# Optimization experiments

Hardware: AMD Instinct MI355X
Metric: run time of the kernel (lower is better)

The kernel has to match this reference:

```python
import jax, jax.numpy as jnp
import numpy as np

B, R, C, E = 4, 32, 512, 512
H = 8
D = E // H  # 64
EPS = 1e-6


def setup_inputs() -> dict:
    key = jax.random.key(0)
    ks = jax.random.split(key, 9)
    s = 1.0 / np.sqrt(E)  # keep activations in a sane range
    return {
        "x": jax.random.normal(ks[0], (B, R, C, E), jnp.float32),
        "Wq": jax.random.normal(ks[1], (E, E), jnp.float32) * s,
        "bq": jax.random.normal(ks[2], (E,), jnp.float32) * 0.01,
        "Wk": jax.random.normal(ks[3], (E, E), jnp.float32) * s,
        "bk": jax.random.normal(ks[4], (E,), jnp.float32) * 0.01,
        "Wv": jax.random.normal(ks[5], (E, E), jnp.float32) * s,
        "bv": jax.random.normal(ks[6], (E,), jnp.float32) * 0.01,
        "Wo": jax.random.normal(ks[7], (E, E), jnp.float32) * s,
        "bo": jax.random.normal(ks[8], (E,), jnp.float32) * 0.01,
    }


def reference(x, Wq, bq, Wk, bk, Wv, bv, Wo, bo):
    b, r, c, e = x.shape
    # projections (torch Linear: y = x @ W.T + b), split heads -> [b,r,c,H,D]
    q = (x @ Wq.T + bq).reshape(b, r, c, H, D)
    k = (x @ Wk.T + bk).reshape(b, r, c, H, D)
    v = (x @ Wv.T + bv).reshape(b, r, c, H, D)
    # ELU+1 feature map (Performer/linear attention)
    q = jax.nn.elu(q) + 1.0
    k = jax.nn.elu(k) + 1.0
    # K^T V accumulation over the column axis: [b,r,H,D,D]
    ktv = jnp.einsum('brchd,brche->brhde', k, v)
    # normalizer: q . sum_c(k)  -> [b,r,c,H]
    ksum = k.sum(axis=2)  # [b,r,H,D]
    z = 1.0 / (jnp.einsum('brchd,brhd->brch', q, ksum) + EPS)
    # O(N) attention output: [b,r,c,H,D]
    out_h = jnp.einsum('brchd,brhde->brche', q, ktv) * z[..., None]
    out = out_h.reshape(b, r, c, e)
    return out @ Wo.T + bo
```

## Files before the change

kernel.cpp:

```cpp
#include <hip/hip_runtime.h>

typedef unsigned short u16;
typedef short short8 __attribute__((ext_vector_type(8)));
typedef float f32x4 __attribute__((ext_vector_type(4)));

__device__ __forceinline__ u16 f2b(float f) {
  unsigned u = __float_as_uint(f);
  u = u + 0x7FFFu + ((u >> 16) & 1u);
  return (u16)(u >> 16);
}
__device__ __forceinline__ float b2f(u16 b) {
  return __uint_as_float(((unsigned)b) << 16);
}

#define ASYNC_LD16(g, l)                                                                   \
  __builtin_amdgcn_global_load_lds((const __attribute__((address_space(1))) void*)(g),     \
                                   (__attribute__((address_space(3))) void*)(l), 16, 0, 0)

#define BAR()                                  \
  do {                                         \
    asm volatile("" ::: "memory");             \
    __builtin_amdgcn_s_barrier();              \
    asm volatile("" ::: "memory");             \
  } while (0)

__global__ void convert_x(const float* __restrict__ x, u16* __restrict__ xb) {
  size_t i = ((size_t)blockIdx.x * 256 + threadIdx.x) * 4;
  float4 f = *(const float4*)(x + i);
  ushort4 o;
  o.x = f2b(f.x); o.y = f2b(f.y); o.z = f2b(f.z); o.w = f2b(f.w);
  *(ushort4*)(xb + i) = o;
}

__global__ void convert_w(const float* __restrict__ Wq, const float* __restrict__ Wk,
                          const float* __restrict__ Wv, const float* __restrict__ Wo,
                          u16* __restrict__ Wqkv, u16* __restrict__ Wob) {
  int idx = (blockIdx.x * 256 + threadIdx.x) * 4;
  int row = idx >> 9;
  int col = idx & 511;
  const float* src = (row < 512)    ? Wq + (size_t)row * 512
                     : (row < 1024) ? Wk + (size_t)(row - 512) * 512
                     : (row < 1536) ? Wv + (size_t)(row - 1024) * 512
                                    : Wo + (size_t)(row - 1536) * 512;
  u16* dst = (row < 1536) ? Wqkv + (size_t)row * 512 : Wob + (size_t)(row - 1536) * 512;
  float4 f = *(const float4*)(src + col);
  ushort4 o;
  o.x = f2b(f.x); o.y = f2b(f.y); o.z = f2b(f.z); o.w = f2b(f.w);
  *(ushort4*)(dst + col) = o;
}


#define LDSV(off) (*(const short8*)&S[(off)])

#define STG(gp, scol, dst)                              \
  do {                                                  \
    ASYNC_LD16((gp) + (scol), S + (dst));               \
    ASYNC_LD16((gp) + (scol) + 4096, S + (dst) + 512);  \
  } while (0)

#define MFMA_CL(MB, JB)                                                                     \
  do {                                                                                      \
    __builtin_amdgcn_s_setprio(1);                                                          \
    _Pragma("unroll") for (int m_ = 0; m_ < 4; ++m_)                                        \
      _Pragma("unroll") for (int j_ = 0; j_ < 2; ++j_) {                                    \
        acc[(MB) + m_][(JB) + j_] = __builtin_amdgcn_mfma_f32_16x16x32_bf16(                \
            aq[m_][0], bf[(JB) + j_][0], acc[(MB) + m_][(JB) + j_], 0, 0, 0);               \
        acc[(MB) + m_][(JB) + j_] = __builtin_amdgcn_mfma_f32_16x16x32_bf16(                \
            aq[m_][1], bf[(JB) + j_][1], acc[(MB) + m_][(JB) + j_], 0, 0, 0);               \
      }                                                                                     \
    __builtin_amdgcn_s_setprio(0);                                                          \
  } while (0)

#define KSTEP(BUF, SG1, SG2, SG3, SG4, BND)                                                  \
  do {                                                                                       \
    short8 aq[4][2], bf[4][2];                                                               \
                                                \
    _Pragma("unroll") for (int m_ = 0; m_ < 4; ++m_) {                                       \
      aq[m_][0] = LDSV((BUF) + rA0 + m_ * 1024);                                             \
      aq[m_][1] = LDSV((BUF) + rA1 + m_ * 1024);                                             \
    }                                                                                        \
    _Pragma("unroll") for (int j_ = 0; j_ < 2; ++j_) {                                       \
      bf[j_][0] = LDSV((BUF) + rB0 + j_ * 1024);                                             \
      bf[j_][1] = LDSV((BUF) + rB1 + j_ * 1024);                                             \
    }                                                                                        \
    SG1;                                                                                     \
    BAR(); MFMA_CL(0, 0); BAR();                                                             \
                                                                    \
    _Pragma("unroll") for (int j_ = 0; j_ < 2; ++j_) {                                       \
      bf[2 + j_][0] = LDSV((BUF) + rB0 + (2 + j_) * 1024);                                   \
      bf[2 + j_][1] = LDSV((BUF) + rB1 + (2 + j_) * 1024);                                   \
    }                                                                                        \
    SG2; BAR(); MFMA_CL(0, 2); BAR();                                                        \
                                  \
    _Pragma("unroll") for (int m_ = 0; m_ < 4; ++m_) {                                       \
      aq[m_][0] = LDSV((BUF) + rA0 + (4 + m_) * 1024);                                       \
      aq[m_][1] = LDSV((BUF) + rA1 + (4 + m_) * 1024);                                       \
    }                                                                                        \
    SG3; BAR(); MFMA_CL(4, 2); BAR();                                                        \
                                                                           \
    SG4; BAR(); MFMA_CL(4, 0); BND; BAR();                                                   \
  } while (0)

#define GEMM8_LOOP()                                                                         \
  STG(gB0, 0, dB0); STG(gB1, 0, dB1);                                                        \
  STG(gA0, 0, dA0); STG(gA1, 0, dA1);                                                        \
  STG(gB0, 64, 32768 + dB0); STG(gB1, 64, 32768 + dB1);                                      \
  asm volatile("s_waitcnt vmcnt(4)" ::: "memory");                                           \
  BAR();                                                                                     \
  _Pragma("unroll") for (int i = 0; i < 4; ++i) {                                            \
    const int s1c = (2 * i + 1) * 64, s2c = (2 * i + 2) * 64, s3c = (2 * i + 3) * 64;        \
    if (i < 3) {                                                                             \
      KSTEP(0,                                                                               \
            STG(gA0, s1c, 32768 + dA0),                                                      \
            STG(gA1, s1c, 32768 + dA1),                                                      \
            STG(gB0, s2c, dB0),                                                              \
            STG(gB1, s2c, dB1),                                                              \
            asm volatile("s_waitcnt vmcnt(4)" ::: "memory"));                                \
      KSTEP(32768,                                                                           \
            STG(gA0, s2c, dA0),                                                              \
            STG(gA1, s2c, dA1),                                                              \
            STG(gB0, s3c, 32768 + dB0),                                                      \
            STG(gB1, s3c, 32768 + dB1),                                                      \
            asm volatile("s_waitcnt vmcnt(4)" ::: "memory"));                                \
    } else {                                                                                 \
      KSTEP(0,                                                                               \
            STG(gA0, s1c, 32768 + dA0),                                                      \
            STG(gA1, s1c, 32768 + dA1),                                                      \
            (void)0, (void)0,                                                                \
            asm volatile("s_waitcnt vmcnt(0)" ::: "memory"));                                \
      KSTEP(32768, (void)0, (void)0, (void)0, (void)0, (void)0);                             \
    }                                                                                        \
  }

__global__ __launch_bounds__(512, 2) void gemm_qkv(
    const u16* __restrict__ xb, const u16* __restrict__ Wqkv,
    const float* __restrict__ bq, const float* __restrict__ bk,
    const float* __restrict__ bv, u16* __restrict__ Qb,
    u16* __restrict__ Ktg, u16* __restrict__ Vtg) {
  __shared__ u16 S[65536];
  const int tid = threadIdx.x;
  const int bid = blockIdx.x;
  const int wg = (bid & 7) * 192 + (bid >> 3);
  const int mtile = wg / 6;
  const int ntile = wg - mtile * 6;
  const int blockM = mtile << 8;
  const int blockN = ntile << 8;

  const int lane = tid & 63;
  const int w = tid >> 6;
  const int wm = (w >> 2) << 7;
  const int wn = (w & 3) << 6;
  const int lr = lane & 15;
  const int qd = lane >> 4;
  const int r7 = lr & 7;
  const int l8 = lane >> 3;
  const int l7 = lane & 7;

  const int gsw8 = (l7 ^ l8) * 8;
  const u16* gA0 = xb + (size_t)(blockM + w * 16 + l8) * 512 + gsw8;
  const u16* gA1 = gA0 + 128 * 512;
  const u16* gB0 = Wqkv + (size_t)(blockN + w * 16 + l8) * 512 + gsw8;
  const u16* gB1 = gB0 + 128 * 512;
  const int dA0 = (w * 16 + l8) * 64 + l7 * 8;
  const int dA1 = dA0 + 8192;
  const int dB0 = dA0 + 16384;
  const int dB1 = dA0 + 24576;

  const int rA0 = (wm + lr) * 64 + ((qd) ^ r7) * 8;
  const int rA1 = (wm + lr) * 64 + ((qd + 4) ^ r7) * 8;
  const int rB0 = 16384 + (wn + lr) * 64 + ((qd) ^ r7) * 8;
  const int rB1 = 16384 + (wn + lr) * 64 + ((qd + 4) ^ r7) * 8;

  f32x4 acc[8][4];
#pragma unroll
  for (int m = 0; m < 8; ++m)
#pragma unroll
    for (int j = 0; j < 4; ++j) acc[m][j] = {0.f, 0.f, 0.f, 0.f};

  GEMM8_LOOP();

  const int which = blockN >> 9;
  const int cb = blockN & 511;
  if (which == 0) {
#pragma unroll
    for (int j = 0; j < 4; ++j) {
      int col = cb + wn + j * 16 + lr;
      float bsv = bq[col];
#pragma unroll
      for (int m = 0; m < 8; ++m) {
        int row = blockM + wm + m * 16 + qd * 4;
#pragma unroll
        for (int r = 0; r < 4; ++r) {
          float v = acc[m][j][r] + bsv;
          v = (v > 0.f) ? v + 1.f : __expf(v);
          Qb[(size_t)(row + r) * 512 + col] = f2b(v);
        }
      }
    }
  } else {
    u16* dstT = (which == 1) ? Ktg : Vtg;
    const float* bias = (which == 1) ? bk : bv;
    const int br = blockM >> 9;
    const int t0 = (blockM & 511) + wm;
#pragma unroll
    for (int j = 0; j < 4; ++j) {
      int col = cb + wn + j * 16 + lr;
      float bsv = bias[col];
      size_t rowbase = (size_t)br * 262144 + (size_t)col * 512;
#pragma unroll
      for (int m = 0; m < 8; ++m) {
        int c0 = t0 + m * 16 + qd * 4;
        float v0 = acc[m][j][0] + bsv, v1 = acc[m][j][1] + bsv;
        float v2 = acc[m][j][2] + bsv, v3 = acc[m][j][3] + bsv;
        if (which == 1) {
          v0 = (v0 > 0.f) ? v0 + 1.f : __expf(v0);
          v1 = (v1 > 0.f) ? v1 + 1.f : __expf(v1);
          v2 = (v2 > 0.f) ? v2 + 1.f : __expf(v2);
          v3 = (v3 > 0.f) ? v3 + 1.f : __expf(v3);
        }
        ushort4 p;
        p.x = f2b(v0); p.y = f2b(v1); p.z = f2b(v2); p.w = f2b(v3);
        *(ushort4*)&dstT[rowbase + c0] = p;
      }
    }
  }
}

__global__ void attn(const u16* __restrict__ Qb, const u16* __restrict__ Ktg,
                     const u16* __restrict__ Vtg, u16* __restrict__ Hb) {
  __shared__ u16 KtS[64 * 32];
  __shared__ u16 VtS[64 * 32];
  __shared__ u16 QS[2 * 128 * 32];
  __shared__ u16 ktvT[2 * 64 * 32];
  __shared__ float part[256];
  __shared__ float ksumf[64];
  __shared__ float zs[128];

  const int tid = threadIdx.x;
  const int br = blockIdx.x >> 3;
  const int h = blockIdx.x & 7;
  const int h64 = h * 64;
  const size_t tok0 = (size_t)br * 512;
  const size_t tbase = (size_t)br * 262144 + (size_t)h64 * 512;

  const int lane = tid & 63;
  const int w = tid >> 6;
  const int lr = lane & 15;
  const int qd = lane >> 4;

  const int sc_chan = tid >> 2, sc_seg = tid & 3;

  f32x4 acc[4];
#pragma unroll
  for (int j = 0; j < 4; ++j) acc[j] = {0.f, 0.f, 0.f, 0.f};
  float ks = 0.f;

  for (int ct = 0; ct < 16; ++ct) {
    __syncthreads();
    {
      size_t g = tbase + (size_t)sc_chan * 512 + ct * 32 + sc_seg * 8;
      ASYNC_LD16(Ktg + g, KtS + tid * 8);
      ASYNC_LD16(Vtg + g, VtS + tid * 8);
    }
    __syncthreads();
    short8 a = *(const short8*)&KtS[(w * 16 + lr) * 32 + qd * 8];
#pragma unroll
    for (int j = 0; j < 4; ++j) {
      short8 b = *(const short8*)&VtS[(j * 16 + lr) * 32 + qd * 8];
      acc[j] = __builtin_amdgcn_mfma_f32_16x16x32_bf16(a, b, acc[j], 0, 0, 0);
    }
    ushort4 k0 = *(const ushort4*)&KtS[sc_chan * 32 + sc_seg * 8];
    ushort4 k1 = *(const ushort4*)&KtS[sc_chan * 32 + sc_seg * 8 + 4];
    ks += b2f(k0.x) + b2f(k0.y) + b2f(k0.z) + b2f(k0.w)
        + b2f(k1.x) + b2f(k1.y) + b2f(k1.z) + b2f(k1.w);
  }
  part[tid] = ks;
  {
    int kc = w >> 1;
    int dp = (w & 1) * 16 + qd * 4;
#pragma unroll
    for (int j = 0; j < 4; ++j) {
      int e = j * 16 + lr;
      ushort4 p;
      p.x = f2b(acc[j][0]); p.y = f2b(acc[j][1]);
      p.z = f2b(acc[j][2]); p.w = f2b(acc[j][3]);
      *(ushort4*)&ktvT[kc * 2048 + e * 32 + dp] = p;
    }
  }
  __syncthreads();
  if (tid < 64)
    ksumf[tid] = part[tid * 4] + part[tid * 4 + 1] + part[tid * 4 + 2] + part[tid * 4 + 3];
  __syncthreads();

  short8 bfr[4][2];
#pragma unroll
  for (int j = 0; j < 4; ++j)
#pragma unroll
    for (int kc = 0; kc < 2; ++kc)
      bfr[j][kc] = *(const short8*)&ktvT[kc * 2048 + (j * 16 + lr) * 32 + qd * 8];

  for (int ct = 0; ct < 4; ++ct) {
    __syncthreads();
#pragma unroll
    for (int kc = 0; kc < 2; ++kc)
#pragma unroll
      for (int half = 0; half < 2; ++half)
        ASYNC_LD16(Qb + (tok0 + ct * 128 + half * 64 + sc_chan) * 512 + h64 + kc * 32 + sc_seg * 8,
                   QS + kc * 4096 + half * 2048 + tid * 8);
    __syncthreads();
    if (tid < 128) {
      float s = 0.f;
#pragma unroll 8
      for (int i = 0; i < 32; ++i) {
        int ix = (i + tid) & 31;
        s += b2f(QS[tid * 32 + ix]) * ksumf[ix];
        s += b2f(QS[4096 + tid * 32 + ix]) * ksumf[32 + ix];
      }
      zs[tid] = 1.f / (s + 1e-6f);
    }
    __syncthreads();
#pragma unroll
    for (int s = 0; s < 2; ++s) {
      int mrow = (w * 2 + s) * 16 + lr;
      short8 a0 = *(const short8*)&QS[mrow * 32 + qd * 8];
      short8 a1 = *(const short8*)&QS[4096 + mrow * 32 + qd * 8];
      f32x4 o[4];
#pragma unroll
      for (int j = 0; j < 4; ++j) {
        o[j] = {0.f, 0.f, 0.f, 0.f};
        o[j] = __builtin_amdgcn_mfma_f32_16x16x32_bf16(a0, bfr[j][0], o[j], 0, 0, 0);
        o[j] = __builtin_amdgcn_mfma_f32_16x16x32_bf16(a1, bfr[j][1], o[j], 0, 0, 0);
      }
      int tl = (w * 2 + s) * 16 + qd * 4;
      float z0 = zs[tl], z1 = zs[tl + 1], z2 = zs[tl + 2], z3 = zs[tl + 3];
      size_t gb = (tok0 + ct * 128 + tl) * 512 + h64;
#pragma unroll
      for (int j = 0; j < 4; ++j) {
        int e = j * 16 + lr;
        Hb[gb + e] = f2b(o[j][0] * z0);
        Hb[gb + 512 + e] = f2b(o[j][1] * z1);
        Hb[gb + 1024 + e] = f2b(o[j][2] * z2);
        Hb[gb + 1536 + e] = f2b(o[j][3] * z3);
      }
    }
  }
}

__global__ __launch_bounds__(512, 2) void gemm_out(
    const u16* __restrict__ Hb, const u16* __restrict__ Wob,
    const float* __restrict__ bo, float* __restrict__ out) {
  __shared__ u16 S[65536];
  const int tid = threadIdx.x;
  const int bid = blockIdx.x;
  const int wg = (bid & 7) * 64 + (bid >> 3);
  const int mtile = wg >> 1;
  const int ntile = wg & 1;
  const int blockM = mtile << 8;
  const int blockN = ntile << 8;

  const int lane = tid & 63;
  const int w = tid >> 6;
  const int wm = (w >> 2) << 7;
  const int wn = (w & 3) << 6;
  const int lr = lane & 15;
  const int qd = lane >> 4;
  const int r7 = lr & 7;
  const int l8 = lane >> 3;
  const int l7 = lane & 7;

  const int gsw8 = (l7 ^ l8) * 8;
  const u16* gA0 = Hb + (size_t)(blockM + w * 16 + l8) * 512 + gsw8;
  const u16* gA1 = gA0 + 128 * 512;
  const u16* gB0 = Wob + (size_t)(blockN + w * 16 + l8) * 512 + gsw8;
  const u16* gB1 = gB0 + 128 * 512;
  const int dA0 = (w * 16 + l8) * 64 + l7 * 8;
  const int dA1 = dA0 + 8192;
  const int dB0 = dA0 + 16384;
  const int dB1 = dA0 + 24576;

  const int rA0 = (wm + lr) * 64 + ((qd) ^ r7) * 8;
  const int rA1 = (wm + lr) * 64 + ((qd + 4) ^ r7) * 8;
  const int rB0 = 16384 + (wn + lr) * 64 + ((qd) ^ r7) * 8;
  const int rB1 = 16384 + (wn + lr) * 64 + ((qd + 4) ^ r7) * 8;

  f32x4 acc[8][4];
#pragma unroll
  for (int m = 0; m < 8; ++m)
#pragma unroll
    for (int j = 0; j < 4; ++j) acc[m][j] = {0.f, 0.f, 0.f, 0.f};

  GEMM8_LOOP();

#pragma unroll
  for (int j = 0; j < 4; ++j) {
    int col = blockN + wn + j * 16 + lr;
    float bsv = bo[col];
#pragma unroll
    for (int m = 0; m < 8; ++m) {
      int row = blockM + wm + m * 16 + qd * 4;
#pragma unroll
      for (int r = 0; r < 4; ++r)
        out[(size_t)(row + r) * 512 + col] = acc[m][j][r] + bsv;
    }
  }
}

extern "C" void kernel_launch(void* const* d_in, const int* in_sizes, int n_in,
                              void* d_out, int out_size, void* d_ws, size_t ws_size,
                              hipStream_t stream) {
  const float* x  = (const float*)d_in[0];
  const float* Wq = (const float*)d_in[1];
  const float* bq = (const float*)d_in[2];
  const float* Wk = (const float*)d_in[3];
  const float* bk = (const float*)d_in[4];
  const float* Wv = (const float*)d_in[5];
  const float* bv = (const float*)d_in[6];
  const float* Wo = (const float*)d_in[7];
  const float* bo = (const float*)d_in[8];
  float* out = (float*)d_out;

  char* ws = (char*)d_ws;
  u16* xb   = (u16*)(ws);
  u16* Wqkv = (u16*)(ws + 0x04000000ull);
  u16* Wob  = (u16*)(ws + 0x04200000ull);
  u16* Qb   = (u16*)(ws + 0x04400000ull);
  u16* Ktg  = (u16*)(ws + 0x08400000ull);
  u16* Vtg  = (u16*)(ws + 0x0C400000ull);
  u16* Hb   = xb;

  hipLaunchKernelGGL(convert_x, dim3(32768), dim3(256), 0, stream, x, xb);
  hipLaunchKernelGGL(convert_w, dim3(1024), dim3(256), 0, stream, Wq, Wk, Wv, Wo, Wqkv, Wob);
  hipLaunchKernelGGL(gemm_qkv, dim3(1536), dim3(512), 0, stream, xb, Wqkv, bq, bk, bv, Qb, Ktg, Vtg);
  hipLaunchKernelGGL(attn, dim3(1024), dim3(256), 0, stream, Qb, Ktg, Vtg, Hb);
  hipLaunchKernelGGL(gemm_out, dim3(512), dim3(512), 0, stream, Hb, Wob, bo, out);
}
```

Before: 465.6 us.

## Pipeline attn kernel: double-buffered V, register-direct K/Q loads, MFMA ksum

Rewrites the attention kernel's K^T V phase. V tiles are now double-buffered in LDS with an XOR swizzle and 64-column chunks, K fragments are loaded straight from global into registers with prefetch, and the K column sum is computed by an MFMA against a ones vector. This replaces the old scalar sum, partial-sum array and two barriers per 32-column step. The Q phase drops LDS staging: Q fragments are loaded directly into registers with prefetch, and the normalizer dot product is done with wave shuffles, removing the per-tile syncthreads. The aim is to cut barrier count and LDS traffic and to overlap global loads with MFMA work. In exchange, the kernel uses more registers and issues uncoalesced direct global loads for K and Q.

```diff
diff --git a/kernel.cpp b/kernel.cpp
--- a/kernel.cpp
+++ b/kernel.cpp
@@ -74,7 +74,6 @@
 #define KSTEP(BUF, SG1, SG2, SG3, SG4, BND)                                                  \
   do {                                                                                       \
     short8 aq[4][2], bf[4][2];                                                               \
-                                                \
     _Pragma("unroll") for (int m_ = 0; m_ < 4; ++m_) {                                       \
       aq[m_][0] = LDSV((BUF) + rA0 + m_ * 1024);                                             \
       aq[m_][1] = LDSV((BUF) + rA1 + m_ * 1024);                                             \
@@ -85,19 +84,16 @@
     }                                                                                        \
     SG1;                                                                                     \
     BAR(); MFMA_CL(0, 0); BAR();                                                             \
-                                                                    \
     _Pragma("unroll") for (int j_ = 0; j_ < 2; ++j_) {                                       \
       bf[2 + j_][0] = LDSV((BUF) + rB0 + (2 + j_) * 1024);                                   \
       bf[2 + j_][1] = LDSV((BUF) + rB1 + (2 + j_) * 1024);                                   \
     }                                                                                        \
     SG2; BAR(); MFMA_CL(0, 2); BAR();                                                        \
-                                  \
     _Pragma("unroll") for (int m_ = 0; m_ < 4; ++m_) {                                       \
       aq[m_][0] = LDSV((BUF) + rA0 + (4 + m_) * 1024);                                       \
       aq[m_][1] = LDSV((BUF) + rA1 + (4 + m_) * 1024);                                       \
     }                                                                                        \
     SG3; BAR(); MFMA_CL(4, 2); BAR();                                                        \
-                                                                           \
     SG4; BAR(); MFMA_CL(4, 0); BND; BAR();                                                   \
   } while (0)
 
@@ -226,15 +222,13 @@
   }
 }
 
-__global__ void attn(const u16* __restrict__ Qb, const u16* __restrict__ Ktg,
-                     const u16* __restrict__ Vtg, u16* __restrict__ Hb) {
-  __shared__ u16 KtS[64 * 32];
-  __shared__ u16 VtS[64 * 32];
-  __shared__ u16 QS[2 * 128 * 32];
+__global__ __launch_bounds__(256) void attn(const u16* __restrict__ Qb,
+                                            const u16* __restrict__ Ktg,
+                                            const u16* __restrict__ Vtg,
+                                            u16* __restrict__ Hb) {
+  __shared__ u16 VtS[2][4096];
   __shared__ u16 ktvT[2 * 64 * 32];
-  __shared__ float part[256];
   __shared__ float ksumf[64];
-  __shared__ float zs[128];
 
   const int tid = threadIdx.x;
   const int br = blockIdx.x >> 3;
@@ -248,33 +242,68 @@
   const int lr = lane & 15;
   const int qd = lane >> 4;
 
-  const int sc_chan = tid >> 2, sc_seg = tid & 3;
+  const int sgi = (tid & 7) ^ ((tid >> 3) & 7);
+  const u16* gV = Vtg + tbase + (size_t)(tid >> 3) * 512 + sgi * 8;
+
+#define STGV(buf, ct)                                              \
+  do {                                                             \
+    ASYNC_LD16(gV + (ct) * 64, &VtS[buf][tid * 8]);                \
+    ASYNC_LD16(gV + 16384 + (ct) * 64, &VtS[buf][2048 + tid * 8]); \
+  } while (0)
+
+  const int g0 = ((qd) ^ (lane & 7)) * 8;
+  const int g1 = ((qd + 4) ^ (lane & 7)) * 8;
+
+  const u16* gK = Ktg + tbase + (size_t)(w * 16 + lr) * 512 + qd * 8;
+
+  short8 ones;
+#pragma unroll
+  for (int i = 0; i < 8; ++i) ones[i] = (short)0x3F80;
 
   f32x4 acc[4];
+  f32x4 aks = {0.f, 0.f, 0.f, 0.f};
 #pragma unroll
   for (int j = 0; j < 4; ++j) acc[j] = {0.f, 0.f, 0.f, 0.f};
-  float ks = 0.f;
-
-  for (int ct = 0; ct < 16; ++ct) {
-    __syncthreads();
-    {
-      size_t g = tbase + (size_t)sc_chan * 512 + ct * 32 + sc_seg * 8;
-      ASYNC_LD16(Ktg + g, KtS + tid * 8);
-      ASYNC_LD16(Vtg + g, VtS + tid * 8);
-    }
-    __syncthreads();
-    short8 a = *(const short8*)&KtS[(w * 16 + lr) * 32 + qd * 8];
-#pragma unroll
-    for (int j = 0; j < 4; ++j) {
-      short8 b = *(const short8*)&VtS[(j * 16 + lr) * 32 + qd * 8];
-      acc[j] = __builtin_amdgcn_mfma_f32_16x16x32_bf16(a, b, acc[j], 0, 0, 0);
-    }
-    ushort4 k0 = *(const ushort4*)&KtS[sc_chan * 32 + sc_seg * 8];
-    ushort4 k1 = *(const ushort4*)&KtS[sc_chan * 32 + sc_seg * 8 + 4];
-    ks += b2f(k0.x) + b2f(k0.y) + b2f(k0.z) + b2f(k0.w)
-        + b2f(k1.x) + b2f(k1.y) + b2f(k1.z) + b2f(k1.w);
-  }
-  part[tid] = ks;
+
+  STGV(0, 0);
+  STGV(1, 1);
+  asm volatile("" ::: "memory");
+  short8 ka0 = *(const short8*)(gK);
+  short8 ka1 = *(const short8*)(gK + 32);
+  asm volatile("s_waitcnt vmcnt(4)" ::: "memory");
+  BAR();
+
+#pragma unroll
+  for (int ct = 0; ct < 8; ++ct) {
+    const int buf = ct & 1;
+    short8 kn0, kn1;
+    if (ct < 7) {
+      kn0 = *(const short8*)(gK + (ct + 1) * 64);
+      kn1 = *(const short8*)(gK + (ct + 1) * 64 + 32);
+    }
+    aks = __builtin_amdgcn_mfma_f32_16x16x32_bf16(ka0, ones, aks, 0, 0, 0);
+#pragma unroll
+    for (int j = 0; j < 4; ++j) {
+      short8 b = *(const short8*)&VtS[buf][(j * 16 + lr) * 64 + g0];
+      acc[j] = __builtin_amdgcn_mfma_f32_16x16x32_bf16(ka0, b, acc[j], 0, 0, 0);
+    }
+    aks = __builtin_amdgcn_mfma_f32_16x16x32_bf16(ka1, ones, aks, 0, 0, 0);
+#pragma unroll
+    for (int j = 0; j < 4; ++j) {
+      short8 b = *(const short8*)&VtS[buf][(j * 16 + lr) * 64 + g1];
+      acc[j] = __builtin_amdgcn_mfma_f32_16x16x32_bf16(ka1, b, acc[j], 0, 0, 0);
+    }
+    BAR();
+    if (ct < 6) {
+      STGV(buf, ct + 2);
+      asm volatile("s_waitcnt vmcnt(4)" ::: "memory");
+    } else if (ct == 6) {
+      asm volatile("s_waitcnt vmcnt(2)" ::: "memory");
+    }
+    BAR();
+    if (ct < 7) { ka0 = kn0; ka1 = kn1; }
+  }
+
   {
     int kc = w >> 1;
     int dp = (w & 1) * 16 + qd * 4;
@@ -287,9 +316,10 @@
       *(ushort4*)&ktvT[kc * 2048 + e * 32 + dp] = p;
     }
   }
-  __syncthreads();
-  if (tid < 64)
-    ksumf[tid] = part[tid * 4] + part[tid * 4 + 1] + part[tid * 4 + 2] + part[tid * 4 + 3];
+  if (lr == 0) {
+#pragma unroll
+    for (int r = 0; r < 4; ++r) ksumf[w * 16 + qd * 4 + r] = aks[r];
+  }
   __syncthreads();
 
   short8 bfr[4][2];
@@ -298,52 +328,57 @@
 #pragma unroll
     for (int kc = 0; kc < 2; ++kc)
       bfr[j][kc] = *(const short8*)&ktvT[kc * 2048 + (j * 16 + lr) * 32 + qd * 8];
-
-  for (int ct = 0; ct < 4; ++ct) {
-    __syncthreads();
-#pragma unroll
-    for (int kc = 0; kc < 2; ++kc)
-#pragma unroll
-      for (int half = 0; half < 2; ++half)
-        ASYNC_LD16(Qb + (tok0 + ct * 128 + half * 64 + sc_chan) * 512 + h64 + kc * 32 + sc_seg * 8,
-                   QS + kc * 4096 + half * 2048 + tid * 8);
-    __syncthreads();
-    if (tid < 128) {
-      float s = 0.f;
-#pragma unroll 8
-      for (int i = 0; i < 32; ++i) {
-        int ix = (i + tid) & 31;
-        s += b2f(QS[tid * 32 + ix]) * ksumf[ix];
-        s += b2f(QS[4096 + tid * 32 + ix]) * ksumf[32 + ix];
-      }
-      zs[tid] = 1.f / (s + 1e-6f);
-    }
-    __syncthreads();
-#pragma unroll
-    for (int s = 0; s < 2; ++s) {
-      int mrow = (w * 2 + s) * 16 + lr;
-      short8 a0 = *(const short8*)&QS[mrow * 32 + qd * 8];
-      short8 a1 = *(const short8*)&QS[4096 + mrow * 32 + qd * 8];
-      f32x4 o[4];
-#pragma unroll
-      for (int j = 0; j < 4; ++j) {
-        o[j] = {0.f, 0.f, 0.f, 0.f};
-        o[j] = __builtin_amdgcn_mfma_f32_16x16x32_bf16(a0, bfr[j][0], o[j], 0, 0, 0);
-        o[j] = __builtin_amdgcn_mfma_f32_16x16x32_bf16(a1, bfr[j][1], o[j], 0, 0, 0);
-      }
-      int tl = (w * 2 + s) * 16 + qd * 4;
-      float z0 = zs[tl], z1 = zs[tl + 1], z2 = zs[tl + 2], z3 = zs[tl + 3];
-      size_t gb = (tok0 + ct * 128 + tl) * 512 + h64;
-#pragma unroll
-      for (int j = 0; j < 4; ++j) {
-        int e = j * 16 + lr;
-        Hb[gb + e] = f2b(o[j][0] * z0);
-        Hb[gb + 512 + e] = f2b(o[j][1] * z1);
-        Hb[gb + 1024 + e] = f2b(o[j][2] * z2);
-        Hb[gb + 1536 + e] = f2b(o[j][3] * z3);
-      }
-    }
-  }
+  float ksf0[8], ksf1[8];
+#pragma unroll
+  for (int i = 0; i < 8; ++i) {
+    ksf0[i] = ksumf[qd * 8 + i];
+    ksf1[i] = ksumf[32 + qd * 8 + i];
+  }
+
+  const u16* gQ = Qb + (tok0 + w * 16 + lr) * 512 + h64 + qd * 8;
+  short8 qa0 = *(const short8*)(gQ);
+  short8 qa1 = *(const short8*)(gQ + 32);
+
+#pragma unroll
+  for (int ct = 0; ct < 8; ++ct) {
+    short8 qn0, qn1;
+    if (ct < 7) {
+      qn0 = *(const short8*)(gQ + (size_t)(ct + 1) * 32768);
+      qn1 = *(const short8*)(gQ + (size_t)(ct + 1) * 32768 + 32);
+    }
+    float dot = 0.f;
+#pragma unroll
+    for (int i = 0; i < 8; ++i) {
+      dot += b2f((u16)qa0[i]) * ksf0[i];
+      dot += b2f((u16)qa1[i]) * ksf1[i];
+    }
+    dot += __shfl_xor(dot, 16);
+    dot += __shfl_xor(dot, 32);
+    float z = 1.f / (dot + 1e-6f);
+
+    f32x4 o[4];
+#pragma unroll
+    for (int j = 0; j < 4; ++j) {
+      o[j] = {0.f, 0.f, 0.f, 0.f};
+      o[j] = __builtin_amdgcn_mfma_f32_16x16x32_bf16(qa0, bfr[j][0], o[j], 0, 0, 0);
+      o[j] = __builtin_amdgcn_mfma_f32_16x16x32_bf16(qa1, bfr[j][1], o[j], 0, 0, 0);
+    }
+    float z0 = __shfl(z, qd * 4 + 0);
+    float z1 = __shfl(z, qd * 4 + 1);
+    float z2 = __shfl(z, qd * 4 + 2);
+    float z3 = __shfl(z, qd * 4 + 3);
+    size_t gb = (tok0 + ct * 64 + w * 16 + qd * 4) * 512 + h64;
+#pragma unroll
+    for (int j = 0; j < 4; ++j) {
+      int e = j * 16 + lr;
+      Hb[gb + e] = f2b(o[j][0] * z0);
+      Hb[gb + 512 + e] = f2b(o[j][1] * z1);
+      Hb[gb + 1024 + e] = f2b(o[j][2] * z2);
+      Hb[gb + 1536 + e] = f2b(o[j][3] * z3);
+    }
+    if (ct < 7) { qa0 = qn0; qa1 = qn1; }
+  }
+#undef STGV
 }
 
 __global__ __launch_bounds__(512, 2) void gemm_out(
```

New measurement: 473.3 us. About the same (+1.7%).
